# Kernel optimization log

Hardware: AMD Instinct MI355X
Metric: run time of the kernel (lower is better)

## Reference

```python
import jax, jax.numpy as jnp
import numpy as np

NDIM = 1024
NTOKEN = 50257
CUTOFFS = [2000, 10000, NTOKEN]  # cutoffs + [ntoken]
DIV = 4
N = 4096
HEAD_SIZE = CUTOFFS[0] + len(CUTOFFS) - 1  # 2002


def setup_inputs() -> dict:
    key = jax.random.key(0)
    ks = jax.random.split(key, 8)
    inputs = jax.random.normal(ks[0], (N, NDIM), dtype=jnp.float32)
    targets = jax.random.randint(ks[1], (N,), 0, NTOKEN, dtype=jnp.int32)
    # head: nn.Linear(ndim, head_size, bias=False) -> weight [head_size, ndim], xavier
    def xavier(k, shape):
        fan_out, fan_in = shape
        lim = np.sqrt(6.0 / (fan_in + fan_out))
        return jax.random.uniform(k, shape, jnp.float32, -lim, lim)
    head_W = xavier(ks[2], (HEAD_SIZE, NDIM))
    # tail cluster 0: size 8000, low dim 256; cluster 1: size 40257, low dim 64
    sz0 = CUTOFFS[1] - CUTOFFS[0]
    sz1 = CUTOFFS[2] - CUTOFFS[1]
    d0, d1 = NDIM // DIV, NDIM // DIV**2
    emb0 = jax.random.normal(ks[3], (sz0, d0), dtype=jnp.float32) * d0 ** -0.5
    emb1 = jax.random.normal(ks[4], (sz1, d1), dtype=jnp.float32) * d1 ** -0.5
    lin0 = xavier(ks[5], (NDIM, d0))  # nn.Linear(d0, ndim).weight
    lin1 = xavier(ks[6], (NDIM, d1))
    return {"inputs": inputs, "targets": targets, "head_W": head_W,
            "emb0": emb0, "lin0": lin0, "emb1": emb1, "lin1": lin1}


def _adaptive_logprob(inputs, targets, head_W, emb0, lin0, emb1, lin1):
    tails = [(emb0, lin0), (emb1, lin1)]
    # map targets -> head targets (in-head id, or cluster slot cutoffs[0]+i)
    head_targets = targets
    masks = []
    for i in range(len(tails)):
        m = (targets >= CUTOFFS[i]) & (targets < CUTOFFS[i + 1])
        masks.append(m)
        head_targets = jnp.where(m, CUTOFFS[0] + i, head_targets)
    # head: logits [N, head_size], gather per-row log-prob
    head_lp = jax.nn.log_softmax(inputs @ head_W.T, axis=-1)
    out = jnp.take_along_axis(head_lp, head_targets[:, None], axis=1)[:, 0]
    # tails: logits = (x @ lin) @ emb^T (low-rank), log-softmax, masked gather
    for i, (emb, lin) in enumerate(tails):
        size = CUTOFFS[i + 1] - CUTOFFS[i]
        lp = jax.nn.log_softmax((inputs @ lin) @ emb.T, axis=-1)  # [N, size]
        rel = jnp.clip(targets - CUTOFFS[i], 0, size - 1)
        g = jnp.take_along_axis(lp, rel[:, None], axis=1)[:, 0]
        out = out + jnp.where(masks[i], g, 0.0)
    return out


def reference(inputs, targets, head_W, emb0, lin0, emb1, lin1):
    outputs = _adaptive_logprob(inputs, targets, head_W, emb0, lin0, emb1, lin1)
    loss = (-outputs).mean()
    return outputs, loss
```

## Files before the change

### kernel.cpp

```cpp
#include <hip/hip_runtime.h>


typedef __attribute__((ext_vector_type(8))) short short8;
typedef __attribute__((ext_vector_type(4))) float f32x4;

#define LOG2E 1.4426950408889634f
#define LN2   0.6931471805599453f

__device__ __forceinline__ float b2f(unsigned short u){
    return __uint_as_float(((unsigned int)u) << 16);
}
__device__ __forceinline__ unsigned short f2b(float f){
    unsigned int x = __float_as_uint(f);
    x += 0x7fffu + ((x >> 16) & 1u);
    return (unsigned short)(x >> 16);
}
__device__ __forceinline__ float dotu(unsigned int xu, unsigned int wu){
    float a = __uint_as_float(xu << 16) * __uint_as_float(wu << 16);
    float b = __uint_as_float(xu & 0xffff0000u) * __uint_as_float(wu & 0xffff0000u);
    return a + b;
}

__global__ __launch_bounds__(256) void k_prep(
    const float* __restrict__ X, const float* __restrict__ headW,
    const float* __restrict__ emb0, const float* __restrict__ emb1,
    const float* __restrict__ lin0, const float* __restrict__ lin1,
    unsigned short* __restrict__ Xb, unsigned short* __restrict__ hWb,
    unsigned short* __restrict__ e0b, unsigned short* __restrict__ e1b,
    unsigned short* __restrict__ l0T, unsigned short* __restrict__ l1T,
    float* __restrict__ sums)
{
    const int NX = 1048576, NH = 512512, NE0 = 512000, NE1 = 644112;
    const int NV = NX + NH + NE0 + NE1;
    const int NT0 = 262144, NT1 = 65536;
    const int NS  = 12288;
    const int total = NV + NT0 + NT1 + NS;
    int stride = gridDim.x * blockDim.x;
    for (int i = blockIdx.x*blockDim.x + threadIdx.x; i < total; i += stride){
        if (i < NV){
            const float* src; unsigned short* dst; int off; float sc;
            if (i < NX)            { src = X;     dst = Xb;  off = i;            sc = 1.0f;  }
            else if (i < NX+NH)    { src = headW; dst = hWb; off = i-NX;         sc = LOG2E; }
            else if (i < NX+NH+NE0){ src = emb0;  dst = e0b; off = i-NX-NH;      sc = LOG2E; }
            else                   { src = emb1;  dst = e1b; off = i-NX-NH-NE0;  sc = LOG2E; }
            float4 v = ((const float4*)src)[off];
            ushort4 o;
            o.x = f2b(v.x*sc); o.y = f2b(v.y*sc);
            o.z = f2b(v.z*sc); o.w = f2b(v.w*sc);
            ((ushort4*)dst)[off] = o;
        } else if (i < NV + NT0){
            int idx = i - NV;
            int c = idx >> 10, d = idx & 1023;
            l0T[idx] = f2b(lin0[d*256 + c]);
        } else if (i < NV + NT0 + NT1){
            int idx = i - NV - NT0;
            int c = idx >> 10, d = idx & 1023;
            l1T[idx] = f2b(lin1[d*64 + c]);
        } else {
            sums[i - NV - NT0 - NT1] = 0.f;
        }
    }
}

__global__ __launch_bounds__(256) void k_hgemm(
    const unsigned short* __restrict__ A,
    const unsigned short* __restrict__ B0, unsigned short* __restrict__ C0,
    const unsigned short* __restrict__ B1, unsigned short* __restrict__ C1)
{
    constexpr int K = 1024;
    __shared__ __align__(16) unsigned short As[64*64];
    __shared__ __align__(16) unsigned short Bs[64*64];

    const int yy = blockIdx.y;
    const unsigned short* B = (yy < 4) ? B0 : B1;
    unsigned short* C = (yy < 4) ? C0 : C1;
    const int M  = (yy < 4) ? 256 : 64;
    const int cb = (yy < 4) ? yy : 0;

    const int tid  = threadIdx.x;
    const int lane = tid & 63;
    const int w    = tid >> 6;
    const int waveR = w >> 1, waveC = w & 1;
    const int quad  = lane >> 4, l16 = lane & 15;
    const int row0  = blockIdx.x * 64;

    f32x4 acc[2][2];
    #pragma unroll
    for (int i = 0; i < 2; ++i)
    #pragma unroll
    for (int j = 0; j < 2; ++j)
        acc[i][j] = (f32x4){0.f, 0.f, 0.f, 0.f};

    for (int kc = 0; kc < K/64; ++kc){
        __syncthreads();
        #pragma unroll
        for (int it = 0; it < 2; ++it){
            int idx = tid + it*256;
            int r = idx >> 3, g = idx & 7;
            *((uint4*)&As[r*64 + ((g ^ (r & 7)) << 3)]) =
                *(const uint4*)(A + (row0 + r)*K + kc*64 + g*8);
            *((uint4*)&Bs[r*64 + ((g ^ (r & 7)) << 3)]) =
                *(const uint4*)(B + (cb*64 + r)*K + kc*64 + g*8);
        }
        __syncthreads();
        #pragma unroll
        for (int ks = 0; ks < 2; ++ks){
            short8 a[2], b[2];
            #pragma unroll
            for (int i = 0; i < 2; ++i){
                int r = waveR*32 + i*16 + l16;
                int g = ks*4 + quad;
                a[i] = *(const short8*)&As[r*64 + ((g ^ (r & 7)) << 3)];
            }
            #pragma unroll
            for (int j = 0; j < 2; ++j){
                int r = waveC*32 + j*16 + l16;
                int g = ks*4 + quad;
                b[j] = *(const short8*)&Bs[r*64 + ((g ^ (r & 7)) << 3)];
            }
            #pragma unroll
            for (int i = 0; i < 2; ++i)
            #pragma unroll
            for (int j = 0; j < 2; ++j)
                acc[i][j] = __builtin_amdgcn_mfma_f32_16x16x32_bf16(
                    a[i], b[j], acc[i][j], 0, 0, 0);
        }
    }
    #pragma unroll
    for (int i = 0; i < 2; ++i)
    #pragma unroll
    for (int j = 0; j < 2; ++j)
    #pragma unroll
    for (int r = 0; r < 4; ++r){
        int row = row0 + waveR*32 + i*16 + quad*4 + r;
        int col = cb*64 + waveC*32 + j*16 + l16;
        C[row*M + col] = f2b(acc[i][j][r]);
    }
}

template<int K>
__device__ __forceinline__ void sumexp_lds(
    const unsigned short* __restrict__ A,
    const unsigned short* __restrict__ B,
    float* __restrict__ s_out, int M,
    int rowb, int cb0, int cb1,
    unsigned short* __restrict__ As,
    unsigned short* __restrict__ Bs)
{
    constexpr int KCH = K / 64;
    constexpr int LK  = (KCH == 16) ? 4 : 2;
    const int tid  = threadIdx.x;
    const int lane = tid & 63, w = tid >> 6;
    const int waveR = w >> 1, waveC = w & 1;
    const int quad  = lane >> 4, l16 = lane & 15;
    const int row0  = rowb * 64;
    const int nit   = (cb1 - cb0) << LK;

    float s_loc[8];
    #pragma unroll
    for (int i = 0; i < 8; ++i) s_loc[i] = 0.f;
    f32x4 acc[2][2];
    #pragma unroll
    for (int i = 0; i < 2; ++i)
    #pragma unroll
    for (int j = 0; j < 2; ++j) acc[i][j] = (f32x4){0.f,0.f,0.f,0.f};

    const int srow = tid >> 3;
    const int sg   = tid & 7;
    const int so0 = srow*64 + ((sg ^ (srow & 7)) << 3);
    const int so1 = (srow+32)*64 + ((sg ^ ((srow+32) & 7)) << 3);

    int aoff[2][2], boff[2][2];
    #pragma unroll
    for (int x = 0; x < 2; ++x)
    #pragma unroll
    for (int ks = 0; ks < 2; ++ks){
        int ra = waveR*32 + x*16 + l16;
        int rb = waveC*32 + x*16 + l16;
        int g  = ks*4 + quad;
        aoff[x][ks] = ra*64 + ((g ^ (ra & 7)) << 3);
        boff[x][ks] = rb*64 + ((g ^ (rb & 7)) << 3);
    }

    uint4 rA0, rA1, rB0, rB1;
    auto loadAB = [&](int it){
        int cb = cb0 + (it >> LK);
        int kc = it & (KCH - 1);
        const unsigned short* ap = A + (row0 + srow)*K + kc*64 + sg*8;
        rA0 = *(const uint4*)ap;
        rA1 = *(const uint4*)(ap + 32*K);
        int br = cb*64 + srow;
        const unsigned short* bp = B + br*K + kc*64 + sg*8;
        rB0 = (br      < M) ? *(const uint4*)bp           : (uint4){0,0,0,0};
        rB1 = (br + 32 < M) ? *(const uint4*)(bp + 32*K)  : (uint4){0,0,0,0};
    };
    auto writeAB = [&](int it){
        unsigned short* Ad = As + (it & 1)*4096;
        unsigned short* Bd = Bs + (it & 1)*4096;
        *(uint4*)(Ad + so0) = rA0;
        *(uint4*)(Ad + so1) = rA1;
        *(uint4*)(Bd + so0) = rB0;
        *(uint4*)(Bd + so1) = rB1;
    };

    loadAB(0);
    writeAB(0);
    if (nit > 1) loadAB(1);
    __syncthreads();

    for (int it = 0; it < nit; ++it){
        if (it + 1 < nit) writeAB(it + 1);
        if (it + 2 < nit) loadAB(it + 2);
        const unsigned short* Ac = As + (it & 1)*4096;
        const unsigned short* Bc = Bs + (it & 1)*4096;
        #pragma unroll
        for (int ks = 0; ks < 2; ++ks){
            short8 a0 = *(const short8*)(Ac + aoff[0][ks]);
            short8 a1 = *(const short8*)(Ac + aoff[1][ks]);
            short8 b0 = *(const short8*)(Bc + boff[0][ks]);
            short8 b1 = *(const short8*)(Bc + boff[1][ks]);
            acc[0][0] = __builtin_amdgcn_mfma_f32_16x16x32_bf16(a0, b0, acc[0][0], 0,0,0);
            acc[0][1] = __builtin_amdgcn_mfma_f32_16x16x32_bf16(a0, b1, acc[0][1], 0,0,0);
            acc[1][0] = __builtin_amdgcn_mfma_f32_16x16x32_bf16(a1, b0, acc[1][0], 0,0,0);
            acc[1][1] = __builtin_amdgcn_mfma_f32_16x16x32_bf16(a1, b1, acc[1][1], 0,0,0);
        }
        if ((it & (KCH - 1)) == (KCH - 1)){
            int cb = cb0 + (it >> LK);
            if ((cb + 1)*64 <= M){
                #pragma unroll
                for (int i = 0; i < 2; ++i)
                #pragma unroll
                for (int j = 0; j < 2; ++j)
                #pragma unroll
                for (int r = 0; r < 4; ++r)
                    s_loc[i*4 + r] += exp2f(acc[i][j][r]);
            } else {
                #pragma unroll
                for (int j = 0; j < 2; ++j){
                    int col = cb*64 + waveC*32 + j*16 + l16;
                    if (col < M){
                        #pragma unroll
                        for (int i = 0; i < 2; ++i)
                        #pragma unroll
                        for (int r = 0; r < 4; ++r)
                            s_loc[i*4 + r] += exp2f(acc[i][j][r]);
                    }
                }
            }
            #pragma unroll
            for (int i = 0; i < 2; ++i)
            #pragma unroll
            for (int j = 0; j < 2; ++j) acc[i][j] = (f32x4){0.f,0.f,0.f,0.f};
        }
        __syncthreads();
    }

    #pragma unroll
    for (int k = 0; k < 8; ++k){
        #pragma unroll
        for (int m = 1; m < 16; m <<= 1)
            s_loc[k] += __shfl_xor(s_loc[k], m, 64);
    }
    if (l16 < 8){
        int i = l16 >> 2, r = l16 & 3;
        int row = row0 + waveR*32 + i*16 + quad*4 + r;
        atomicAdd(&s_out[row], s_loc[l16]);
    }
}

__device__ __forceinline__ void sumexp_stream64(
    const unsigned short* __restrict__ A,
    const unsigned short* __restrict__ B,
    float* __restrict__ s_out, int wid)
{
    const int M = 40257;
    const int lane = threadIdx.x & 63;
    const int quad = lane >> 4, l16 = lane & 15;
    const int rowg  = wid >> 6;
    const int split = wid & 63;
    const int g0 = split*39 + min(split, 21);
    const int g1 = g0 + 39 + (split < 21 ? 1 : 0);
    const int row0 = rowg * 128;

    short8 a[8][2];
    #pragma unroll
    for (int i = 0; i < 8; ++i)
    #pragma unroll
    for (int ks = 0; ks < 2; ++ks)
        a[i][ks] = *(const short8*)(A + (row0 + i*16 + l16)*64 + ks*32 + quad*8);

    f32x4 sums[8];
    #pragma unroll
    for (int i = 0; i < 8; ++i) sums[i] = (f32x4){0.f,0.f,0.f,0.f};

    short8 bcur0, bcur1, bnxt0, bnxt1;
    auto loadB = [&](int g, short8& d0, short8& d1){
        int n = g*16 + l16; if (n > M-1) n = M-1;
        const unsigned short* p = B + n*64 + quad*8;
        d0 = *(const short8*)p;
        d1 = *(const short8*)(p + 32);
    };
    loadB(g0, bcur0, bcur1);
    for (int g = g0; g < g1; ++g){
        if (g + 1 < g1) loadB(g + 1, bnxt0, bnxt1);
        f32x4 acc[8];
        #pragma unroll
        for (int i = 0; i < 8; ++i) acc[i] = (f32x4){0.f,0.f,0.f,0.f};
        #pragma unroll
        for (int i = 0; i < 8; ++i)
            acc[i] = __builtin_amdgcn_mfma_f32_16x16x32_bf16(a[i][0], bcur0, acc[i], 0,0,0);
        #pragma unroll
        for (int i = 0; i < 8; ++i)
            acc[i] = __builtin_amdgcn_mfma_f32_16x16x32_bf16(a[i][1], bcur1, acc[i], 0,0,0);
        if (g*16 + l16 < M){
            #pragma unroll
            for (int i = 0; i < 8; ++i){
                sums[i][0] += exp2f(acc[i][0]);
                sums[i][1] += exp2f(acc[i][1]);
                sums[i][2] += exp2f(acc[i][2]);
                sums[i][3] += exp2f(acc[i][3]);
            }
        }
        bcur0 = bnxt0; bcur1 = bnxt1;
    }

    #pragma unroll
    for (int i = 0; i < 8; ++i){
        #pragma unroll
        for (int r = 0; r < 4; ++r){
            float v = sums[i][r];
            v += __shfl_xor(v, 1, 64);
            v += __shfl_xor(v, 2, 64);
            v += __shfl_xor(v, 4, 64);
            v += __shfl_xor(v, 8, 64);
            if (l16 == 0)
                atomicAdd(&s_out[row0 + i*16 + quad*4 + r], v);
        }
    }
}

__global__ __launch_bounds__(256) void k_sumexp(
    const unsigned short* __restrict__ Xb,  const unsigned short* __restrict__ hWb,
    const unsigned short* __restrict__ h0b, const unsigned short* __restrict__ e0b,
    const unsigned short* __restrict__ h1b, const unsigned short* __restrict__ e1b,
    float* __restrict__ sH, float* __restrict__ s0, float* __restrict__ s1)
{
    __shared__ __align__(16) unsigned short As[2*4096];
    __shared__ __align__(16) unsigned short Bs[2*4096];
    const int b = blockIdx.x;
    if (b < 512){
        int rowb = b >> 3, split = b & 7;
        sumexp_lds<1024>(Xb, hWb, sH, 2002, rowb, split*4, split*4 + 4, As, Bs);
    } else if (b < 1024){
        int bb = b - 512;
        int rowb = bb >> 3, split = bb & 7;
        int cb0 = split*16, cb1 = min(125, cb0 + 16);
        sumexp_lds<256>(h0b, e0b, s0, 8000, rowb, cb0, cb1, As, Bs);
    } else {
        int wid = (b - 1024)*4 + (threadIdx.x >> 6);
        sumexp_stream64(h1b, e1b, s1, wid);
    }
}

__global__ __launch_bounds__(256) void k_combine(
    const unsigned short* __restrict__ Xb,
    const unsigned short* __restrict__ hWb,
    const unsigned short* __restrict__ h0b,
    const unsigned short* __restrict__ e0b,
    const unsigned short* __restrict__ h1b,
    const unsigned short* __restrict__ e1b,
    const float* __restrict__ sH, const float* __restrict__ s0,
    const float* __restrict__ s1,
    const int* __restrict__ targets, float* __restrict__ out)
{
    int w = threadIdx.x >> 6, lane = threadIdx.x & 63;
    int row = blockIdx.x*4 + w;
    int t = targets[row];
    int hidx = t < 2000 ? t : (t < 10000 ? 2000 : 2001);
    int rel0 = min(max(t - 2000, 0), 7999);
    int rel1 = min(max(t - 10000, 0), 40256);

    float dh = 0.f;
    {
        const uint4* xa = (const uint4*)(Xb  + row*1024  + lane*16);
        const uint4* wb = (const uint4*)(hWb + hidx*1024 + lane*16);
        #pragma unroll
        for (int p = 0; p < 2; ++p){
            uint4 xv = xa[p], wv = wb[p];
            dh += dotu(xv.x, wv.x) + dotu(xv.y, wv.y)
                + dotu(xv.z, wv.z) + dotu(xv.w, wv.w);
        }
    }
    float d0;
    {
        uint2 xv = *(const uint2*)(h0b + row*256  + lane*4);
        uint2 wv = *(const uint2*)(e0b + rel0*256 + lane*4);
        d0 = dotu(xv.x, wv.x) + dotu(xv.y, wv.y);
    }
    float d1 = b2f(h1b[row*64 + lane]) * b2f(e1b[rel1*64 + lane]);

    #pragma unroll
    for (int m = 1; m < 64; m <<= 1){
        dh += __shfl_xor(dh, m, 64);
        d0 += __shfl_xor(d0, m, 64);
        d1 += __shfl_xor(d1, m, 64);
    }
    if (lane == 0){
        float lp = dh - log2f(sH[row]);
        if (t >= 2000 && t < 10000) lp += d0 - log2f(s0[row]);
        if (t >= 10000)             lp += d1 - log2f(s1[row]);
        out[row] = LN2 * lp;
    }
}

__global__ void k_loss(const float* __restrict__ out, float* __restrict__ loss){
    __shared__ float red[1024];
    float s = 0.f;
    for (int i = threadIdx.x; i < 4096; i += 1024) s += out[i];
    red[threadIdx.x] = s;
    __syncthreads();
    for (int ofs = 512; ofs > 0; ofs >>= 1){
        if (threadIdx.x < ofs) red[threadIdx.x] += red[threadIdx.x + ofs];
        __syncthreads();
    }
    if (threadIdx.x == 0) loss[0] = -red[0] / 4096.f;
}

extern "C" void kernel_launch(void* const* d_in, const int* in_sizes, int n_in,
                              void* d_out, int out_size, void* d_ws, size_t ws_size,
                              hipStream_t stream) {
    const float* X      = (const float*)d_in[0];
    const int*   tgt    = (const int*)  d_in[1];
    const float* headW  = (const float*)d_in[2];
    const float* emb0   = (const float*)d_in[3];
    const float* lin0   = (const float*)d_in[4];
    const float* emb1   = (const float*)d_in[5];
    const float* lin1   = (const float*)d_in[6];
    float* out = (float*)d_out;

    char* ws = (char*)d_ws;
    unsigned short* Xb  = (unsigned short*)(ws + 0);
    unsigned short* hWb = (unsigned short*)(ws + 8388608);
    unsigned short* e0b = (unsigned short*)(ws + 12488704);
    unsigned short* e1b = (unsigned short*)(ws + 16584704);
    unsigned short* l0T = (unsigned short*)(ws + 21737600);
    unsigned short* l1T = (unsigned short*)(ws + 22261888);
    unsigned short* h0b = (unsigned short*)(ws + 22392960);
    unsigned short* h1b = (unsigned short*)(ws + 24490112);
    float* sums         = (float*)(ws + 25014400);
    float* sH = sums, *s0 = sums + 4096, *s1 = sums + 8192;

    k_prep<<<2048, 256, 0, stream>>>(X, headW, emb0, emb1, lin0, lin1,
                                     Xb, hWb, e0b, e1b, l0T, l1T, sums);
    k_hgemm<<<dim3(64, 5), 256, 0, stream>>>(Xb, l0T, h0b, l1T, h1b);
    k_sumexp<<<1536, 256, 0, stream>>>(Xb, hWb, h0b, e0b, h1b, e1b, sH, s0, s1);
    k_combine<<<1024, 256, 0, stream>>>(Xb, hWb, h0b, e0b, h1b, e1b,
                                        sH, s0, s1, tgt, out);
    k_loss<<<1, 1024, 0, stream>>>(out, out + 4096);
}
```

Measured before the change: 290.8 us.

## Rebalance sumexp work interleaving, deepen prefetch, tile lin transpose, use fast exp2

Replaces the strided lin0/lin1 transpose in k_prep with an LDS-tiled transpose done by 80 dedicated blocks. In sumexp_lds, the loop is unrolled by two with a two-stage register prefetch (ping-pong buffers) so loads run further ahead of the MFMA work. sumexp_stream64 now processes 64 rows per wave instead of 128, with a two-deep B prefetch. k_sumexp interleaves head, tail0 and tail1 blocks by blockIdx modulo 4 and balances the tail0 column splits; the grid grows to 2048 blocks. exp2f is replaced with the hardware v_exp_f32 intrinsic. The risks are lower precision from the raw exp and more register pressure. Halving rows per wave also means the B stream for tail1 is read twice as many times.

```diff
diff --git a/kernel.cpp b/kernel.cpp
--- a/kernel.cpp
+++ b/kernel.cpp
@@ -19,6 +19,13 @@
     float a = __uint_as_float(xu << 16) * __uint_as_float(wu << 16);
     float b = __uint_as_float(xu & 0xffff0000u) * __uint_as_float(wu & 0xffff0000u);
     return a + b;
+}
+__device__ __forceinline__ float fexp2(float x){
+#if __has_builtin(__builtin_amdgcn_exp2f)
+    return __builtin_amdgcn_exp2f(x);
+#else
+    float r; asm("v_exp_f32 %0, %1" : "=v"(r) : "v"(x)); return r;
+#endif
 }
 
 __global__ __launch_bounds__(256) void k_prep(
@@ -30,34 +37,44 @@
     unsigned short* __restrict__ l0T, unsigned short* __restrict__ l1T,
     float* __restrict__ sums)
 {
+    __shared__ unsigned short tileT[64][65];
+    const int b = blockIdx.x, t = threadIdx.x;
+    if (b < 80){
+        const float* src; unsigned short* dst; int C, tx, ty;
+        if (b < 64){ src = lin0; dst = l0T; C = 256; tx = b & 3; ty = b >> 2; }
+        else       { src = lin1; dst = l1T; C = 64;  tx = 0;     ty = b - 64; }
+        #pragma unroll
+        for (int e = 0; e < 16; ++e){
+            int idx = t + e*256, r = idx >> 6, c = idx & 63;
+            tileT[c][r] = f2b(src[(ty*64 + r)*C + tx*64 + c]);
+        }
+        __syncthreads();
+        #pragma unroll
+        for (int e = 0; e < 16; ++e){
+            int idx = t + e*256, cc = idx >> 6, rr = idx & 63;
+            dst[(tx*64 + cc)*1024 + ty*64 + rr] = tileT[cc][rr];
+        }
+        return;
+    }
     const int NX = 1048576, NH = 512512, NE0 = 512000, NE1 = 644112;
     const int NV = NX + NH + NE0 + NE1;
-    const int NT0 = 262144, NT1 = 65536;
-    const int NS  = 12288;
-    const int total = NV + NT0 + NT1 + NS;
-    int stride = gridDim.x * blockDim.x;
-    for (int i = blockIdx.x*blockDim.x + threadIdx.x; i < total; i += stride){
+    const int NS = 12288;
+    const int total = NV + NS;
+    int stride = (gridDim.x - 80) * blockDim.x;
+    for (int i = (b - 80)*blockDim.x + t; i < total; i += stride){
         if (i < NV){
             const float* src; unsigned short* dst; int off; float sc;
-            if (i < NX)            { src = X;     dst = Xb;  off = i;            sc = 1.0f;  }
-            else if (i < NX+NH)    { src = headW; dst = hWb; off = i-NX;         sc = LOG2E; }
-            else if (i < NX+NH+NE0){ src = emb0;  dst = e0b; off = i-NX-NH;      sc = LOG2E; }
-            else                   { src = emb1;  dst = e1b; off = i-NX-NH-NE0;  sc = LOG2E; }
+            if (i < NX)            { src = X;     dst = Xb;  off = i;           sc = 1.0f;  }
+            else if (i < NX+NH)    { src = headW; dst = hWb; off = i-NX;        sc = LOG2E; }
+            else if (i < NX+NH+NE0){ src = emb0;  dst = e0b; off = i-NX-NH;     sc = LOG2E; }
+            else                   { src = emb1;  dst = e1b; off = i-NX-NH-NE0; sc = LOG2E; }
             float4 v = ((const float4*)src)[off];
             ushort4 o;
             o.x = f2b(v.x*sc); o.y = f2b(v.y*sc);
             o.z = f2b(v.z*sc); o.w = f2b(v.w*sc);
             ((ushort4*)dst)[off] = o;
-        } else if (i < NV + NT0){
-            int idx = i - NV;
-            int c = idx >> 10, d = idx & 1023;
-            l0T[idx] = f2b(lin0[d*256 + c]);
-        } else if (i < NV + NT0 + NT1){
-            int idx = i - NV - NT0;
-            int c = idx >> 10, d = idx & 1023;
-            l1T[idx] = f2b(lin1[d*64 + c]);
         } else {
-            sums[i - NV - NT0 - NT1] = 0.f;
+            sums[i - NV] = 0.f;
         }
     }
 }
@@ -149,6 +166,7 @@
 {
     constexpr int KCH = K / 64;
     constexpr int LK  = (KCH == 16) ? 4 : 2;
+    static_assert(KCH == 16 || KCH == 4, "");
     const int tid  = threadIdx.x;
     const int lane = tid & 63, w = tid >> 6;
     const int waveR = w >> 1, waveC = w & 1;
@@ -182,37 +200,27 @@
         boff[x][ks] = rb*64 + ((g ^ (rb & 7)) << 3);
     }
 
-    uint4 rA0, rA1, rB0, rB1;
-    auto loadAB = [&](int it){
+    uint4 A0a, A1a, B0a, B1a, A0b, A1b, B0b, B1b;
+    auto loadAB = [&](int it, uint4& A0, uint4& A1, uint4& B0, uint4& B1){
         int cb = cb0 + (it >> LK);
         int kc = it & (KCH - 1);
         const unsigned short* ap = A + (row0 + srow)*K + kc*64 + sg*8;
-        rA0 = *(const uint4*)ap;
-        rA1 = *(const uint4*)(ap + 32*K);
+        A0 = *(const uint4*)ap;
+        A1 = *(const uint4*)(ap + 32*K);
         int br = cb*64 + srow;
         const unsigned short* bp = B + br*K + kc*64 + sg*8;
-        rB0 = (br      < M) ? *(const uint4*)bp           : (uint4){0,0,0,0};
-        rB1 = (br + 32 < M) ? *(const uint4*)(bp + 32*K)  : (uint4){0,0,0,0};
-    };
-    auto writeAB = [&](int it){
+        B0 = (br      < M) ? *(const uint4*)bp          : (uint4){0,0,0,0};
+        B1 = (br + 32 < M) ? *(const uint4*)(bp + 32*K) : (uint4){0,0,0,0};
+    };
+    auto writeAB = [&](int it, uint4 A0, uint4 A1, uint4 B0, uint4 B1){
         unsigned short* Ad = As + (it & 1)*4096;
         unsigned short* Bd = Bs + (it & 1)*4096;
-        *(uint4*)(Ad + so0) = rA0;
-        *(uint4*)(Ad + so1) = rA1;
-        *(uint4*)(Bd + so0) = rB0;
-        *(uint4*)(Bd + so1) = rB1;
-    };
-
-    loadAB(0);
-    writeAB(0);
-    if (nit > 1) loadAB(1);
-    __syncthreads();
-
-    for (int it = 0; it < nit; ++it){
-        if (it + 1 < nit) writeAB(it + 1);
-        if (it + 2 < nit) loadAB(it + 2);
-        const unsigned short* Ac = As + (it & 1)*4096;
-        const unsigned short* Bc = Bs + (it & 1)*4096;
+        *(uint4*)(Ad + so0) = A0; *(uint4*)(Ad + so1) = A1;
+        *(uint4*)(Bd + so0) = B0; *(uint4*)(Bd + so1) = B1;
+    };
+    auto compute = [&](int buf){
+        const unsigned short* Ac = As + buf*4096;
+        const unsigned short* Bc = Bs + buf*4096;
         #pragma unroll
         for (int ks = 0; ks < 2; ++ks){
             short8 a0 = *(const short8*)(Ac + aoff[0][ks]);
@@ -224,34 +232,51 @@
             acc[1][0] = __builtin_amdgcn_mfma_f32_16x16x32_bf16(a1, b0, acc[1][0], 0,0,0);
             acc[1][1] = __builtin_amdgcn_mfma_f32_16x16x32_bf16(a1, b1, acc[1][1], 0,0,0);
         }
-        if ((it & (KCH - 1)) == (KCH - 1)){
-            int cb = cb0 + (it >> LK);
-            if ((cb + 1)*64 <= M){
-                #pragma unroll
-                for (int i = 0; i < 2; ++i)
-                #pragma unroll
-                for (int j = 0; j < 2; ++j)
-                #pragma unroll
-                for (int r = 0; r < 4; ++r)
-                    s_loc[i*4 + r] += exp2f(acc[i][j][r]);
-            } else {
-                #pragma unroll
-                for (int j = 0; j < 2; ++j){
-                    int col = cb*64 + waveC*32 + j*16 + l16;
-                    if (col < M){
-                        #pragma unroll
-                        for (int i = 0; i < 2; ++i)
-                        #pragma unroll
-                        for (int r = 0; r < 4; ++r)
-                            s_loc[i*4 + r] += exp2f(acc[i][j][r]);
-                    }
+    };
+    auto epilogue = [&](int it){
+        int cb = cb0 + (it >> LK);
+        if ((cb + 1)*64 <= M){
+            #pragma unroll
+            for (int i = 0; i < 2; ++i)
+            #pragma unroll
+            for (int j = 0; j < 2; ++j)
+            #pragma unroll
+            for (int r = 0; r < 4; ++r)
+                s_loc[i*4 + r] += fexp2(acc[i][j][r]);
+        } else {
+            #pragma unroll
+            for (int j = 0; j < 2; ++j){
+                int col = cb*64 + waveC*32 + j*16 + l16;
+                if (col < M){
+                    #pragma unroll
+                    for (int i = 0; i < 2; ++i)
+                    #pragma unroll
+                    for (int r = 0; r < 4; ++r)
+                        s_loc[i*4 + r] += fexp2(acc[i][j][r]);
                 }
             }
-            #pragma unroll
-            for (int i = 0; i < 2; ++i)
-            #pragma unroll
-            for (int j = 0; j < 2; ++j) acc[i][j] = (f32x4){0.f,0.f,0.f,0.f};
-        }
+        }
+        #pragma unroll
+        for (int i = 0; i < 2; ++i)
+        #pragma unroll
+        for (int j = 0; j < 2; ++j) acc[i][j] = (f32x4){0.f,0.f,0.f,0.f};
+    };
+
+    loadAB(0, A0a, A1a, B0a, B1a);
+    writeAB(0, A0a, A1a, B0a, B1a);
+    loadAB(1, A0b, A1b, B0b, B1b);
+    loadAB(2, A0a, A1a, B0a, B1a);
+    __syncthreads();
+
+    for (int it = 0; it < nit; it += 2){
+        writeAB(it + 1, A0b, A1b, B0b, B1b);
+        if (it + 3 < nit) loadAB(it + 3, A0b, A1b, B0b, B1b);
+        compute(0);
+        __syncthreads();
+        if (it + 2 < nit) writeAB(it + 2, A0a, A1a, B0a, B1a);
+        if (it + 4 < nit) loadAB(it + 4, A0a, A1a, B0a, B1a);
+        compute(1);
+        if (((it + 1) & (KCH - 1)) == (KCH - 1)) epilogue(it + 1);
         __syncthreads();
     }
 
@@ -280,52 +305,60 @@
     const int split = wid & 63;
     const int g0 = split*39 + min(split, 21);
     const int g1 = g0 + 39 + (split < 21 ? 1 : 0);
-    const int row0 = rowg * 128;
-
-    short8 a[8][2];
-    #pragma unroll
-    for (int i = 0; i < 8; ++i)
+    const int row0 = rowg * 64;
+
+    short8 a[4][2];
+    #pragma unroll
+    for (int i = 0; i < 4; ++i)
     #pragma unroll
     for (int ks = 0; ks < 2; ++ks)
         a[i][ks] = *(const short8*)(A + (row0 + i*16 + l16)*64 + ks*32 + quad*8);
 
-    f32x4 sums[8];
-    #pragma unroll
-    for (int i = 0; i < 8; ++i) sums[i] = (f32x4){0.f,0.f,0.f,0.f};
-
-    short8 bcur0, bcur1, bnxt0, bnxt1;
+    f32x4 sums[4];
+    #pragma unroll
+    for (int i = 0; i < 4; ++i) sums[i] = (f32x4){0.f,0.f,0.f,0.f};
+
+    short8 p0a, p1a, p0b, p1b;
     auto loadB = [&](int g, short8& d0, short8& d1){
         int n = g*16 + l16; if (n > M-1) n = M-1;
         const unsigned short* p = B + n*64 + quad*8;
         d0 = *(const short8*)p;
         d1 = *(const short8*)(p + 32);
     };
-    loadB(g0, bcur0, bcur1);
-    for (int g = g0; g < g1; ++g){
-        if (g + 1 < g1) loadB(g + 1, bnxt0, bnxt1);
-        f32x4 acc[8];
-        #pragma unroll
-        for (int i = 0; i < 8; ++i) acc[i] = (f32x4){0.f,0.f,0.f,0.f};
-        #pragma unroll
-        for (int i = 0; i < 8; ++i)
-            acc[i] = __builtin_amdgcn_mfma_f32_16x16x32_bf16(a[i][0], bcur0, acc[i], 0,0,0);
-        #pragma unroll
-        for (int i = 0; i < 8; ++i)
-            acc[i] = __builtin_amdgcn_mfma_f32_16x16x32_bf16(a[i][1], bcur1, acc[i], 0,0,0);
+    auto body = [&](int g, short8 b0, short8 b1){
+        f32x4 acc[4];
+        #pragma unroll
+        for (int i = 0; i < 4; ++i) acc[i] = (f32x4){0.f,0.f,0.f,0.f};
+        #pragma unroll
+        for (int i = 0; i < 4; ++i)
+            acc[i] = __builtin_amdgcn_mfma_f32_16x16x32_bf16(a[i][0], b0, acc[i], 0,0,0);
+        #pragma unroll
+        for (int i = 0; i < 4; ++i)
+            acc[i] = __builtin_amdgcn_mfma_f32_16x16x32_bf16(a[i][1], b1, acc[i], 0,0,0);
         if (g*16 + l16 < M){
             #pragma unroll
-            for (int i = 0; i < 8; ++i){
-                sums[i][0] += exp2f(acc[i][0]);
-                sums[i][1] += exp2f(acc[i][1]);
-                sums[i][2] += exp2f(acc[i][2]);
-                sums[i][3] += exp2f(acc[i][3]);
+            for (int i = 0; i < 4; ++i){
+                sums[i][0] += fexp2(acc[i][0]);
+                sums[i][1] += fexp2(acc[i][1]);
+                sums[i][2] += fexp2(acc[i][2]);
+                sums[i][3] += fexp2(acc[i][3]);
             }
         }
-        bcur0 = bnxt0; bcur1 = bnxt1;
-    }
-
-    #pragma unroll
-    for (int i = 0; i < 8; ++i){
+    };
+
+    loadB(g0, p0a, p1a);
+    loadB(g0 + 1, p0b, p1b);
+    for (int g = g0; g < g1; g += 2){
+        body(g, p0a, p1a);
+        if (g + 2 < g1) loadB(g + 2, p0a, p1a);
+        if (g + 1 < g1){
+            body(g + 1, p0b, p1b);
+            if (g + 3 < g1) loadB(g + 3, p0b, p1b);
+        }
+    }
+
+    #pragma unroll
+    for (int i = 0; i < 4; ++i){
         #pragma unroll
         for (int r = 0; r < 4; ++r){
             float v = sums[i][r];
@@ -348,16 +381,17 @@
     __shared__ __align__(16) unsigned short As[2*4096];
     __shared__ __align__(16) unsigned short Bs[2*4096];
     const int b = blockIdx.x;
-    if (b < 512){
-        int rowb = b >> 3, split = b & 7;
+    const int m4 = b & 3;
+    if (m4 == 0){
+        int id = b >> 2, rowb = id >> 3, split = id & 7;
         sumexp_lds<1024>(Xb, hWb, sH, 2002, rowb, split*4, split*4 + 4, As, Bs);
-    } else if (b < 1024){
-        int bb = b - 512;
-        int rowb = bb >> 3, split = bb & 7;
-        int cb0 = split*16, cb1 = min(125, cb0 + 16);
+    } else if (m4 == 2){
+        int id = b >> 2, rowb = id >> 3, split = id & 7;
+        int cb0 = split*15 + min(split, 5);
+        int cb1 = cb0 + 15 + (split < 5 ? 1 : 0);
         sumexp_lds<256>(h0b, e0b, s0, 8000, rowb, cb0, cb1, As, Bs);
     } else {
-        int wid = (b - 1024)*4 + (threadIdx.x >> 6);
+        int wid = (b >> 1)*4 + (threadIdx.x >> 6);
         sumexp_stream64(h1b, e1b, s1, wid);
     }
 }
@@ -453,7 +487,7 @@
     k_prep<<<2048, 256, 0, stream>>>(X, headW, emb0, emb1, lin0, lin1,
                                      Xb, hWb, e0b, e1b, l0T, l1T, sums);
     k_hgemm<<<dim3(64, 5), 256, 0, stream>>>(Xb, l0T, h0b, l1T, h1b);
-    k_sumexp<<<1536, 256, 0, stream>>>(Xb, hWb, h0b, e0b, h1b, e1b, sH, s0, s1);
+    k_sumexp<<<2048, 256, 0, stream>>>(Xb, hWb, h0b, e0b, h1b, e1b, sH, s0, s1);
     k_combine<<<1024, 256, 0, stream>>>(Xb, hWb, h0b, e0b, h1b, e1b,
                                         sH, s0, s1, tgt, out);
     k_loss<<<1, 1024, 0, stream>>>(out, out + 4096);
```

Result: faster. 234.2 us (-19.5%).
